# Kernel tuning notes

Hardware: AMD Instinct MI355X
Metric: run time of the kernel (lower is better)

## Reference

```python
import jax, jax.numpy as jnp
import numpy as np

N = 100000      # nodes
E = 3200000     # edges (avg degree 32)
FEA = 67
HID = 16
OUT = 2
K = 3           # num_stacks
T = 2           # num_layers


def setup_inputs() -> dict:
    key = jax.random.key(0)
    ks = jax.random.split(key, 11)
    s = 0.1  # weight init scale
    return {
        "x": jax.random.normal(ks[0], (N, FEA), jnp.float32),
        "edge_index": jax.random.randint(ks[1], (2, E), 0, N, dtype=jnp.int32),
        "init_w1": jax.random.normal(ks[2], (K, FEA, HID), jnp.float32) * s,
        "w1": jax.random.normal(ks[3], (1, K, HID, HID), jnp.float32) * s,
        "root_w1": jax.random.normal(ks[4], (1, K, FEA, HID), jnp.float32) * s,
        "b1": jax.random.normal(ks[5], (1, K, 1, HID), jnp.float32) * s,
        "init_w2": jax.random.normal(ks[6], (K, HID, OUT), jnp.float32) * s,
        "w2": jax.random.normal(ks[7], (1, K, OUT, OUT), jnp.float32) * s,
        "root_w2": jax.random.normal(ks[8], (1, K, HID, OUT), jnp.float32) * s,
        "b2": jax.random.normal(ks[9], (1, K, 1, OUT), jnp.float32) * s,
    }


def gcn_norm(src, dst, n):
    # symmetric normalization of A WITHOUT self-loops (PyG ARMAConv behavior)
    deg = jax.ops.segment_sum(jnp.ones(src.shape[0], jnp.float32), dst, num_segments=n)
    dinv = jnp.where(deg > 0, jax.lax.rsqrt(jnp.maximum(deg, 1.0)), 0.0)
    return dinv[src] * dinv[dst]  # [E]


def arma_conv(x, src, dst, norm, init_w, w, root_w, bias, act, n):
    # x: [N, Fin]; shared_weights=True, num_layers=T, num_stacks=K
    out = jnp.einsum('nf,kfh->knh', x, init_w)           # t=0 transform
    root = jnp.einsum('nf,kfh->knh', x, root_w[0])       # root term (dropout=identity in eval)
    for t in range(T):
        if t > 0:
            out = jnp.einsum('knh,khp->knp', out, w[0])
        # propagate: out[i] = sum_{(j->i)} norm_e * out[j]
        m = (out[:, src, :] * norm[None, :, None]).transpose(1, 0, 2)  # [E,K,H]
        agg = jax.ops.segment_sum(m, dst, num_segments=n).transpose(1, 0, 2)  # [K,N,H]
        out = agg + root + bias[0]
        if act:
            out = jax.nn.relu(out)
    return out.mean(axis=0)  # average over stacks -> [N, H]


def reference(x, edge_index, init_w1, w1, root_w1, b1, init_w2, w2, root_w2, b2):
    src, dst = edge_index[0], edge_index[1]
    n = x.shape[0]
    norm = gcn_norm(src, dst, n)
    h = jax.nn.relu(arma_conv(x, src, dst, norm, init_w1, w1, root_w1, b1, True, n))
    o = arma_conv(h, src, dst, norm, init_w2, w2, root_w2, b2, False, n)
    return jax.nn.log_softmax(o, axis=1)
```

## Files before the change

### kernel.cpp

```cpp
#include <hip/hip_runtime.h>
#include <hip/hip_fp16.h>
#include <math.h>

#define NN 100000
#define NE 3200000
#define FEA 67
#define HID 16
#define OUTC 2
#define KS 3
#define KH 48
#define KO 6
#define PAD 64

#define PB 512
#define EPB 6250
#define BINW 512
#define NBINS 196
#define M1 (NBINS * PB)
#define NSCB 98
#define CSR_CAP (NE + NBINS * 3 * BINW + 64)

#define TBM 128
#define TNB ((NN + TBM - 1) / TBM)
#define XS_STRIDE 132
#define WT_STRIDE 68


__global__ void k_hist(const int* __restrict__ dst, int* __restrict__ hist) {
    __shared__ int h[NBINS];
    if (threadIdx.x < NBINS) h[threadIdx.x] = 0;
    __syncthreads();
    int base = blockIdx.x * EPB;
    for (int i = threadIdx.x; i < EPB; i += 256)
        atomicAdd(&h[dst[base + i] >> 9], 1);
    __syncthreads();
    if (threadIdx.x < NBINS) hist[threadIdx.x * PB + blockIdx.x] = h[threadIdx.x];
}


__global__ void k_partial(const int* __restrict__ in, int* __restrict__ partials, int n) {
    __shared__ int s[256];
    int base = blockIdx.x * 1024;
    int acc = 0;
    for (int i = threadIdx.x; i < 1024; i += 256) {
        int idx = base + i;
        if (idx < n) acc += in[idx];
    }
    s[threadIdx.x] = acc;
    __syncthreads();
    for (int off = 128; off > 0; off >>= 1) {
        if (threadIdx.x < off) s[threadIdx.x] += s[threadIdx.x + off];
        __syncthreads();
    }
    if (threadIdx.x == 0) partials[blockIdx.x] = s[0];
}

__global__ void k_downsweepF(const int* __restrict__ in, const int* __restrict__ partials,
                             int* __restrict__ out, int n) {
    __shared__ int ps[256];
    __shared__ int s[256];
    int t = threadIdx.x;
    ps[t] = (t < NSCB) ? partials[t] : 0;
    __syncthreads();
    for (int off = 1; off < 256; off <<= 1) {
        int v = (t >= off) ? ps[t - off] : 0;
        __syncthreads();
        ps[t] += v;
        __syncthreads();
    }
    int bbase = (blockIdx.x > 0) ? ps[blockIdx.x - 1] : 0;

    int base = blockIdx.x * 1024 + t * 4;
    int d0 = 0, d1 = 0, d2 = 0, d3 = 0;
    if (base + 0 < n) d0 = in[base + 0];
    if (base + 1 < n) d1 = in[base + 1];
    if (base + 2 < n) d2 = in[base + 2];
    if (base + 3 < n) d3 = in[base + 3];
    int ts = d0 + d1 + d2 + d3;
    s[t] = ts;
    __syncthreads();
    for (int off = 1; off < 256; off <<= 1) {
        int v = (t >= off) ? s[t - off] : 0;
        __syncthreads();
        s[t] += v;
        __syncthreads();
    }
    int excl = s[t] - ts + bbase;
    if (base + 0 < n) out[base + 0] = excl;
    if (base + 1 < n) out[base + 1] = excl + d0;
    if (base + 2 < n) out[base + 2] = excl + d0 + d1;
    if (base + 3 < n) out[base + 3] = excl + d0 + d1 + d2;
}


__global__ void k_pass2(const int* __restrict__ src, const int* __restrict__ dst,
                        const int* __restrict__ hist_scan, int* __restrict__ recs) {
    __shared__ int curs[NBINS];
    if (threadIdx.x < NBINS) curs[threadIdx.x] = hist_scan[threadIdx.x * PB + blockIdx.x];
    __syncthreads();
    int base = blockIdx.x * EPB;
    for (int i = threadIdx.x; i < EPB; i += 256) {
        int e = base + i;
        int s = src[e], d = dst[e];
        int pos = atomicAdd(&curs[d >> 9], 1);
        recs[pos] = s | ((d & 511) << 17);
    }
}


__global__ void k_degsort(const int* __restrict__ recs, const int* __restrict__ hist_scan,
                          int* __restrict__ deg, float* __restrict__ dinv,
                          int* __restrict__ row_start, int* __restrict__ csr) {
    __shared__ int cnt[BINW];
    __shared__ int scn[BINW];
    int bin = blockIdx.x, t = threadIdx.x;
    cnt[t] = 0;
    __syncthreads();
    int s0 = hist_scan[bin * PB];
    int s1 = (bin + 1 < NBINS) ? hist_scan[(bin + 1) * PB] : NE;
    for (int r = s0 + t; r < s1; r += BINW)
        atomicAdd(&cnt[((unsigned)recs[r]) >> 17], 1);
    __syncthreads();
    int c  = cnt[t];
    int c4 = (c + 3) & ~3;
    scn[t] = c4;
    __syncthreads();
    for (int off = 1; off < BINW; off <<= 1) {
        int v = (t >= off) ? scn[t - off] : 0;
        __syncthreads();
        scn[t] += v;
        __syncthreads();
    }
    int base = s0 + bin * (3 * BINW);
    int rs   = base + scn[t] - c4;
    int node = bin * BINW + t;
    if (node < NN) {
        deg[node]       = c;
        dinv[node]      = (c > 0) ? rsqrtf((float)c) : 0.f;
        row_start[node] = rs;
    }
    scn[t] = rs;
    __syncthreads();
    for (int r = s0 + t; r < s1; r += BINW) {
        int rec = recs[r];
        int pos = atomicAdd(&scn[((unsigned)rec) >> 17], 1);
        csr[pos] = rec & 0x1FFFF;
    }
    __syncthreads();
    int e4 = rs + c4;
    for (int i = scn[t]; i < e4; ++i) csr[i] = NN;
}


__global__ void k_transform1(const float* __restrict__ x, const float* __restrict__ iw,
                             const float* __restrict__ rw, const float* __restrict__ b1,
                             const float* __restrict__ dinv,
                             __half* __restrict__ A, __half* __restrict__ Bpad,
                             __half2* __restrict__ Rh) {
    if (blockIdx.x == TNB) {
        int t = threadIdx.x;
        if (t < PAD) A[(size_t)NN * PAD + t] = __float2half(0.f);
        else if (t < 2 * PAD) Bpad[(size_t)NN * PAD + (t - PAD)] = __float2half(0.f);
        return;
    }
    __shared__ float xs[FEA * XS_STRIDE];
    __shared__ float wTs[96 * WT_STRIDE];
    __shared__ float bb[KH];
    int n0g = blockIdx.x * TBM;

    for (int idx = threadIdx.x; idx < 96 * FEA; idx += 256) {
        int j = idx / FEA, f = idx % FEA;
        float v;
        if (j < KH) v = iw[(j >> 4) * (FEA * HID) + f * HID + (j & 15)];
        else { int jr = j - KH; v = rw[(jr >> 4) * (FEA * HID) + f * HID + (jr & 15)]; }
        wTs[j * WT_STRIDE + f] = v;
    }
    if (threadIdx.x < KH) bb[threadIdx.x] = b1[threadIdx.x];
    for (int idx = threadIdx.x; idx < TBM * FEA; idx += 256) {
        int nl = idx / FEA, f = idx % FEA;
        int n = n0g + nl;
        xs[f * XS_STRIDE + nl] = (n < NN) ? x[(size_t)n * FEA + f] : 0.f;
    }
    __syncthreads();

    int tx = threadIdx.x & 31, ty = threadIdx.x >> 5;
    int nl0 = tx * 4;
    int j0  = ty * 12;
    float acc[4][12];
    #pragma unroll
    for (int p = 0; p < 12; ++p) {
        float init = (j0 >= KH) ? bb[j0 - KH + p] : 0.f;
        acc[0][p] = init; acc[1][p] = init; acc[2][p] = init; acc[3][p] = init;
    }

    #pragma unroll 4
    for (int fb = 0; fb < 16; ++fb) {
        int f0 = fb * 4;
        float4 xv0 = *(const float4*)&xs[(f0 + 0) * XS_STRIDE + nl0];
        float4 xv1 = *(const float4*)&xs[(f0 + 1) * XS_STRIDE + nl0];
        float4 xv2 = *(const float4*)&xs[(f0 + 2) * XS_STRIDE + nl0];
        float4 xv3 = *(const float4*)&xs[(f0 + 3) * XS_STRIDE + nl0];
        #pragma unroll
        for (int p = 0; p < 12; ++p) {
            float4 wv = *(const float4*)&wTs[(j0 + p) * WT_STRIDE + f0];
            acc[0][p] += xv0.x * wv.x + xv1.x * wv.y + xv2.x * wv.z + xv3.x * wv.w;
            acc[1][p] += xv0.y * wv.x + xv1.y * wv.y + xv2.y * wv.z + xv3.y * wv.w;
            acc[2][p] += xv0.z * wv.x + xv1.z * wv.y + xv2.z * wv.z + xv3.z * wv.w;
            acc[3][p] += xv0.w * wv.x + xv1.w * wv.y + xv2.w * wv.z + xv3.w * wv.w;
        }
    }
    #pragma unroll
    for (int f = 64; f < FEA; ++f) {
        float x0 = xs[f * XS_STRIDE + nl0 + 0];
        float x1 = xs[f * XS_STRIDE + nl0 + 1];
        float x2 = xs[f * XS_STRIDE + nl0 + 2];
        float x3 = xs[f * XS_STRIDE + nl0 + 3];
        #pragma unroll
        for (int p = 0; p < 12; ++p) {
            float wv = wTs[(j0 + p) * WT_STRIDE + f];
            acc[0][p] += x0 * wv; acc[1][p] += x1 * wv;
            acc[2][p] += x2 * wv; acc[3][p] += x3 * wv;
        }
    }

    if (j0 < KH) {
        #pragma unroll
        for (int nq = 0; nq < 4; ++nq) {
            int n = n0g + nl0 + nq;
            if (n < NN) {
                float dv = dinv[n];
                __half2* Ap = (__half2*)A + (size_t)n * (PAD / 2) + (j0 >> 1);
                #pragma unroll
                for (int p2 = 0; p2 < 6; ++p2)
                    Ap[p2] = __halves2half2(__float2half_rn(acc[nq][2 * p2] * dv),
                                            __float2half_rn(acc[nq][2 * p2 + 1] * dv));
            }
        }
    } else {
        int jh = (j0 - KH) >> 1;
        #pragma unroll
        for (int nq = 0; nq < 4; ++nq) {
            int n = n0g + nl0 + nq;
            if (n < NN) {
                __half2* Rp = Rh + (size_t)n * 24 + jh;
                #pragma unroll
                for (int p2 = 0; p2 < 6; ++p2)
                    Rp[p2] = __halves2half2(__float2half_rn(acc[nq][2 * p2]),
                                            __float2half_rn(acc[nq][2 * p2 + 1]));
            }
        }
    }
}


template <bool FUSEW>
__global__ void k_spmm48(const __half2* __restrict__ Asrc,
                         const __half2* __restrict__ Rh,
                         const int* __restrict__ row_start, const int* __restrict__ deg,
                         const float* __restrict__ dinv, const int* __restrict__ csr,
                         const float* __restrict__ w1, __half2* __restrict__ Bout) {
    __shared__ float w1s[FUSEW ? KS * HID * HID : 1];
    if (FUSEW) {
        for (int i = threadIdx.x; i < KS * HID * HID; i += 256) w1s[i] = w1[i];
        __syncthreads();
    }
    int node = (blockIdx.x * 256 + threadIdx.x) >> 6;
    int lane = threadIdx.x & 63;
    int eo   = lane >> 5;
    int cl   = lane & 31;
    int start = __builtin_amdgcn_readfirstlane(row_start[node]);
    int d     = __builtin_amdgcn_readfirstlane(deg[node]);
    int d4    = (d + 3) & ~3;
    float dv  = dinv[node];
    float2 r2 = make_float2(0.f, 0.f);
    if (cl < 24) r2 = __half22float2(Rh[(size_t)node * 24 + cl]);

    float ax = 0.f, ay = 0.f;
    for (int b = 0; b < d4; b += 64) {
        int nb  = min(64, d4 - b);
        int myc = csr[start + b + lane];
        int npf = nb >> 1;
        int p = 0;
        for (; p + 4 <= npf; p += 4) {
            int c0 = __shfl(myc, 2 * (p + 0) + eo, 64);
            int c1 = __shfl(myc, 2 * (p + 1) + eo, 64);
            int c2 = __shfl(myc, 2 * (p + 2) + eo, 64);
            int c3 = __shfl(myc, 2 * (p + 3) + eo, 64);
            float2 f0 = __half22float2(Asrc[(size_t)c0 * (PAD / 2) + cl]);
            float2 f1 = __half22float2(Asrc[(size_t)c1 * (PAD / 2) + cl]);
            float2 f2 = __half22float2(Asrc[(size_t)c2 * (PAD / 2) + cl]);
            float2 f3 = __half22float2(Asrc[(size_t)c3 * (PAD / 2) + cl]);
            ax += f0.x + f1.x; ay += f0.y + f1.y;
            ax += f2.x + f3.x; ay += f2.y + f3.y;
        }
        for (; p < npf; ++p) {
            int c = __shfl(myc, 2 * p + eo, 64);
            float2 f = __half22float2(Asrc[(size_t)c * (PAD / 2) + cl]);
            ax += f.x; ay += f.y;
        }
    }
    ax += __shfl_xor(ax, 32, 64);
    ay += __shfl_xor(ay, 32, 64);
    float vx = fmaxf(ax * dv + r2.x, 0.f);
    float vy = fmaxf(ay * dv + r2.y, 0.f);

    if (FUSEW) {
        int k  = cl >> 3;
        int p0 = (2 * cl) & 15;
        float o0 = 0.f, o1 = 0.f;
        #pragma unroll
        for (int h2 = 0; h2 < 8; ++h2) {
            float ix = __shfl(vx, k * 8 + h2, 64);
            float iy = __shfl(vy, k * 8 + h2, 64);
            o0 += ix * w1s[k * 256 + (2 * h2) * 16 + p0]     + iy * w1s[k * 256 + (2 * h2 + 1) * 16 + p0];
            o1 += ix * w1s[k * 256 + (2 * h2) * 16 + p0 + 1] + iy * w1s[k * 256 + (2 * h2 + 1) * 16 + p0 + 1];
        }
        if (eo == 0 && cl < 24)
            Bout[(size_t)node * (PAD / 2) + cl] =
                __halves2half2(__float2half_rn(o0 * dv), __float2half_rn(o1 * dv));
    } else {
        if (eo == 0 && cl < 24)
            Bout[(size_t)node * (PAD / 2) + cl] =
                __halves2half2(__float2half_rn(vx), __float2half_rn(vy));
    }
}


__global__ void k_mt2(const __half* __restrict__ L1, const float* __restrict__ iw,
                      const float* __restrict__ rw, const float* __restrict__ b2,
                      const float* __restrict__ dinv,
                      float* __restrict__ A2, float* __restrict__ R2) {
    __shared__ float wi[KS * HID * OUTC];
    __shared__ float wr_[KS * HID * OUTC];
    __shared__ float bb[KO];
    if (threadIdx.x < KS * HID * OUTC) { wi[threadIdx.x] = iw[threadIdx.x]; wr_[threadIdx.x] = rw[threadIdx.x]; }
    if (threadIdx.x < KO) bb[threadIdx.x] = b2[threadIdx.x];
    __syncthreads();
    int n = blockIdx.x * 256 + threadIdx.x;
    if (n >= NN) return;
    const __half2* hp = (const __half2*)(L1 + (size_t)n * PAD);
    float v[KH];
    #pragma unroll
    for (int q = 0; q < 24; ++q) {
        float2 f = __half22float2(hp[q]);
        v[q * 2 + 0] = f.x; v[q * 2 + 1] = f.y;
    }
    float h[HID];
    #pragma unroll
    for (int hh = 0; hh < HID; ++hh)
        h[hh] = fmaxf((v[hh] + v[16 + hh] + v[32 + hh]) * (1.f / 3.f), 0.f);
    float dv = dinv[n];
    #pragma unroll
    for (int k = 0; k < KS; ++k) {
        #pragma unroll
        for (int o = 0; o < OUTC; ++o) {
            float a = 0.f, r = bb[k * 2 + o];
            #pragma unroll
            for (int hh = 0; hh < HID; ++hh) {
                a += h[hh] * wi[k * 32 + hh * 2 + o];
                r += h[hh] * wr_[k * 32 + hh * 2 + o];
            }
            A2[n * KO + k * 2 + o] = a * dv;
            R2[n * KO + k * 2 + o] = r;
        }
    }
}


__global__ void k_spmm6_g(const float* __restrict__ Asrc, const float* __restrict__ R2,
                          const int* __restrict__ row_start, const int* __restrict__ deg,
                          const float* __restrict__ dinv, const int* __restrict__ csr,
                          const float* __restrict__ w2, float* __restrict__ Bout) {
    __shared__ float ws[KS * OUTC * OUTC];
    if (threadIdx.x < KS * OUTC * OUTC) ws[threadIdx.x] = w2[threadIdx.x];
    __syncthreads();
    int t = blockIdx.x * 256 + threadIdx.x;
    int node = t / KO, j = t % KO;
    bool active = node < NN;
    float acc = 0.f, r = 0.f, dv = 0.f;
    int start = 0, d = 0;
    if (active) {
        start = row_start[node];
        d     = deg[node];
        r     = R2[node * KO + j];
        dv    = dinv[node];
    }
    int e = 0;
    for (; e + 4 <= d; e += 4) {
        int c0 = csr[start + e + 0];
        int c1 = csr[start + e + 1];
        int c2 = csr[start + e + 2];
        int c3 = csr[start + e + 3];
        acc += Asrc[c0 * KO + j];
        acc += Asrc[c1 * KO + j];
        acc += Asrc[c2 * KO + j];
        acc += Asrc[c3 * KO + j];
    }
    for (; e < d; ++e)
        acc += Asrc[csr[start + e] * KO + j];
    float v = acc * dv + r;
    float other = __shfl_xor(v, 1, 64);
    if (active) {
        int k = j >> 1, p = j & 1;
        float v0 = (p == 0) ? v : other;
        float v1 = (p == 0) ? other : v;
        Bout[node * KO + j] = (v0 * ws[k * 4 + p] + v1 * ws[k * 4 + 2 + p]) * dv;
    }
}


__global__ void k_spmm6_f(const float* __restrict__ Asrc, const float* __restrict__ R2,
                          const int* __restrict__ row_start, const int* __restrict__ deg,
                          const float* __restrict__ dinv, const int* __restrict__ csr,
                          float* __restrict__ out) {
    int wave = threadIdx.x >> 6;
    int l    = threadIdx.x & 63;
    int nl   = l / 6;
    int j    = l - nl * 6;
    bool active = nl < 10;
    int node = blockIdx.x * 40 + wave * 10 + nl;
    float acc = 0.f, r = 0.f, dv = 0.f;
    int start = 0, d = 0;
    if (active) {
        start = row_start[node];
        d     = deg[node];
        r     = R2[node * KO + j];
        dv    = dinv[node];
    }
    int e = 0;
    for (; e + 4 <= d; e += 4) {
        int c0 = csr[start + e + 0];
        int c1 = csr[start + e + 1];
        int c2 = csr[start + e + 2];
        int c3 = csr[start + e + 3];
        acc += Asrc[c0 * KO + j];
        acc += Asrc[c1 * KO + j];
        acc += Asrc[c2 * KO + j];
        acc += Asrc[c3 * KO + j];
    }
    for (; e < d; ++e)
        acc += Asrc[csr[start + e] * KO + j];
    float v = acc * dv + r;
    int base = nl * 6;
    float o0 = (__shfl(v, base + 0, 64) + __shfl(v, base + 2, 64) + __shfl(v, base + 4, 64)) * (1.f / 3.f);
    float o1 = (__shfl(v, base + 1, 64) + __shfl(v, base + 3, 64) + __shfl(v, base + 5, 64)) * (1.f / 3.f);
    if (active && j == 0) {
        float m = fmaxf(o0, o1);
        float ls = m + logf(expf(o0 - m) + expf(o1 - m));
        *(float2*)(out + (size_t)node * 2) = make_float2(o0 - ls, o1 - ls);
    }
}


extern "C" void kernel_launch(void* const* d_in, const int* in_sizes, int n_in,
                              void* d_out, int out_size, void* d_ws, size_t ws_size,
                              hipStream_t stream) {
    const float* x   = (const float*)d_in[0];
    const int*   ei  = (const int*)d_in[1];
    const float* iw1 = (const float*)d_in[2];
    const float* w1  = (const float*)d_in[3];
    const float* rw1 = (const float*)d_in[4];
    const float* b1  = (const float*)d_in[5];
    const float* iw2 = (const float*)d_in[6];
    const float* w2  = (const float*)d_in[7];
    const float* rw2 = (const float*)d_in[8];
    const float* b2  = (const float*)d_in[9];
    const int* src = ei;
    const int* dst = ei + NE;
    float* out = (float*)d_out;

    char* ws = (char*)d_ws;
    size_t o = 0;
    int*     deg       = (int*)(ws + o);     o += (size_t)NN * 4;
    int*     row_start = (int*)(ws + o);     o += (size_t)NN * 4;
    float*   dinv      = (float*)(ws + o);   o += (size_t)NN * 4;
    int*     hist      = (int*)(ws + o);     o += (size_t)M1 * 4;
    int*     hist_scan = (int*)(ws + o);     o += (size_t)M1 * 4;
    int*     partials  = (int*)(ws + o);     o += 128 * 4;
    int*     csr       = (int*)(ws + o);     o += (size_t)CSR_CAP * 4;
    __half*  A         = (__half*)(ws + o);  o += (size_t)(NN + 1) * PAD * 2;
    __half2* Rh        = (__half2*)(ws + o); o += (size_t)NN * 24 * 4;
    __half*  B         = (__half*)(ws + o);  o += (size_t)(NN + 1) * PAD * 2;
    int*    recs  = (int*)A;
    __half* L1f   = A;
    float*  A2    = (float*)Rh;
    float*  R2    = (float*)Rh + (size_t)NN * KO;
    float*  C2    = (float*)Rh + (size_t)NN * KO * 2;

    k_hist       <<<PB, 256, 0, stream>>>(dst, hist);
    k_partial    <<<NSCB, 256, 0, stream>>>(hist, partials, M1);
    k_downsweepF <<<NSCB, 256, 0, stream>>>(hist, partials, hist_scan, M1);
    k_pass2      <<<PB, 256, 0, stream>>>(src, dst, hist_scan, recs);
    k_degsort    <<<NBINS, BINW, 0, stream>>>(recs, hist_scan, deg, dinv, row_start, csr);

    k_transform1    <<<TNB + 1, 256, 0, stream>>>(x, iw1, rw1, b1, dinv, A, B, Rh);
    k_spmm48<true>  <<<NN / 4, 256, 0, stream>>>((const __half2*)A, Rh, row_start, deg, dinv, csr, w1, (__half2*)B);
    k_spmm48<false> <<<NN / 4, 256, 0, stream>>>((const __half2*)B, Rh, row_start, deg, dinv, csr, w1, (__half2*)L1f);

    k_mt2      <<<(NN + 255) / 256, 256, 0, stream>>>(L1f, iw2, rw2, b2, dinv, A2, R2);
    k_spmm6_g  <<<(NN * KO + 255) / 256, 256, 0, stream>>>(A2, R2, row_start, deg, dinv, csr, w2, C2);
    k_spmm6_f  <<<NN / 40, 256, 0, stream>>>(C2, R2, row_start, deg, dinv, csr, out);
}
```

Baseline: 324.0 us.

## Split layer-1 features into per-stack planar arrays and run SpMM per stack

Replaces the 64-half padded per-node layout holding all three stacks with three planar 16-half arrays, and launches the first-layer SpMM once per stack with 8 lanes per neighbour and 8 neighbours per step. CSR rows are padded to multiples of 8 to match. This removes the wasted padding lanes and shrinks the per-launch gather working set for better cache hit rates, at the cost of traversing the CSR three times and more kernel launches.

```diff
diff --git a/kernel.cpp b/kernel.cpp
--- a/kernel.cpp
+++ b/kernel.cpp
@@ -10,7 +10,6 @@
 #define KS 3
 #define KH 48
 #define KO 6
-#define PAD 64
 
 #define PB 512
 #define EPB 6250
@@ -18,12 +17,15 @@
 #define NBINS 196
 #define M1 (NBINS * PB)
 #define NSCB 98
-#define CSR_CAP (NE + NBINS * 3 * BINW + 64)
+#define CSR_CAP (NE + NBINS * 7 * BINW + 64)
 
 #define TBM 128
 #define TNB ((NN + TBM - 1) / TBM)
 #define XS_STRIDE 132
 #define WT_STRIDE 68
+
+#define APS ((size_t)(NN + 1) * 8)
+#define RPS ((size_t)NN * 8)
 
 
 __global__ void k_hist(const int* __restrict__ dst, int* __restrict__ hist) {
@@ -122,8 +124,8 @@
         atomicAdd(&cnt[((unsigned)recs[r]) >> 17], 1);
     __syncthreads();
     int c  = cnt[t];
-    int c4 = (c + 3) & ~3;
-    scn[t] = c4;
+    int c8 = (c + 7) & ~7;
+    scn[t] = c8;
     __syncthreads();
     for (int off = 1; off < BINW; off <<= 1) {
         int v = (t >= off) ? scn[t - off] : 0;
@@ -131,8 +133,8 @@
         scn[t] += v;
         __syncthreads();
     }
-    int base = s0 + bin * (3 * BINW);
-    int rs   = base + scn[t] - c4;
+    int base = s0 + bin * (7 * BINW);
+    int rs   = base + scn[t] - c8;
     int node = bin * BINW + t;
     if (node < NN) {
         deg[node]       = c;
@@ -147,20 +149,21 @@
         csr[pos] = rec & 0x1FFFF;
     }
     __syncthreads();
-    int e4 = rs + c4;
-    for (int i = scn[t]; i < e4; ++i) csr[i] = NN;
+    int e8 = rs + c8;
+    for (int i = scn[t]; i < e8; ++i) csr[i] = NN;
 }
 
 
 __global__ void k_transform1(const float* __restrict__ x, const float* __restrict__ iw,
                              const float* __restrict__ rw, const float* __restrict__ b1,
                              const float* __restrict__ dinv,
-                             __half* __restrict__ A, __half* __restrict__ Bpad,
-                             __half2* __restrict__ Rh) {
+                             __half2* __restrict__ Ap, __half2* __restrict__ Bp,
+                             __half2* __restrict__ Rp) {
     if (blockIdx.x == TNB) {
         int t = threadIdx.x;
-        if (t < PAD) A[(size_t)NN * PAD + t] = __float2half(0.f);
-        else if (t < 2 * PAD) Bpad[(size_t)NN * PAD + (t - PAD)] = __float2half(0.f);
+        __half2 z = __halves2half2(__float2half(0.f), __float2half(0.f));
+        if (t < 24)      Ap[(size_t)(t >> 3) * APS + (size_t)NN * 8 + (t & 7)] = z;
+        else if (t < 48) Bp[(size_t)((t - 24) >> 3) * APS + (size_t)NN * 8 + ((t - 24) & 7)] = z;
         return;
     }
     __shared__ float xs[FEA * XS_STRIDE];
@@ -229,24 +232,28 @@
             int n = n0g + nl0 + nq;
             if (n < NN) {
                 float dv = dinv[n];
-                __half2* Ap = (__half2*)A + (size_t)n * (PAD / 2) + (j0 >> 1);
                 #pragma unroll
-                for (int p2 = 0; p2 < 6; ++p2)
-                    Ap[p2] = __halves2half2(__float2half_rn(acc[nq][2 * p2] * dv),
-                                            __float2half_rn(acc[nq][2 * p2 + 1] * dv));
+                for (int p2 = 0; p2 < 6; ++p2) {
+                    int jp = j0 + 2 * p2;
+                    Ap[(size_t)(jp >> 4) * APS + (size_t)n * 8 + ((jp & 15) >> 1)] =
+                        __halves2half2(__float2half_rn(acc[nq][2 * p2] * dv),
+                                       __float2half_rn(acc[nq][2 * p2 + 1] * dv));
+                }
             }
         }
     } else {
-        int jh = (j0 - KH) >> 1;
+        int jr0 = j0 - KH;
         #pragma unroll
         for (int nq = 0; nq < 4; ++nq) {
             int n = n0g + nl0 + nq;
             if (n < NN) {
-                __half2* Rp = Rh + (size_t)n * 24 + jh;
                 #pragma unroll
-                for (int p2 = 0; p2 < 6; ++p2)
-                    Rp[p2] = __halves2half2(__float2half_rn(acc[nq][2 * p2]),
-                                            __float2half_rn(acc[nq][2 * p2 + 1]));
+                for (int p2 = 0; p2 < 6; ++p2) {
+                    int jp = jr0 + 2 * p2;
+                    Rp[(size_t)(jp >> 4) * RPS + (size_t)n * 8 + ((jp & 15) >> 1)] =
+                        __halves2half2(__float2half_rn(acc[nq][2 * p2]),
+                                       __float2half_rn(acc[nq][2 * p2 + 1]));
+                }
             }
         }
     }
@@ -254,79 +261,79 @@
 
 
 template <bool FUSEW>
-__global__ void k_spmm48(const __half2* __restrict__ Asrc,
-                         const __half2* __restrict__ Rh,
+__global__ void k_spmm16(const __half2* __restrict__ Ak,
+                         const __half2* __restrict__ Rk,
                          const int* __restrict__ row_start, const int* __restrict__ deg,
                          const float* __restrict__ dinv, const int* __restrict__ csr,
-                         const float* __restrict__ w1, __half2* __restrict__ Bout) {
-    __shared__ float w1s[FUSEW ? KS * HID * HID : 1];
+                         const float* __restrict__ w1k,
+                         __half2* __restrict__ Bk) {
+    __shared__ float w1s[FUSEW ? HID * HID : 1];
     if (FUSEW) {
-        for (int i = threadIdx.x; i < KS * HID * HID; i += 256) w1s[i] = w1[i];
+        if (threadIdx.x < HID * HID) w1s[threadIdx.x] = w1k[threadIdx.x];
         __syncthreads();
     }
     int node = (blockIdx.x * 256 + threadIdx.x) >> 6;
     int lane = threadIdx.x & 63;
-    int eo   = lane >> 5;
-    int cl   = lane & 31;
+    int eo   = lane >> 3;
+    int cl   = lane & 7;
     int start = __builtin_amdgcn_readfirstlane(row_start[node]);
     int d     = __builtin_amdgcn_readfirstlane(deg[node]);
-    int d4    = (d + 3) & ~3;
+    int d8    = (d + 7) & ~7;
     float dv  = dinv[node];
-    float2 r2 = make_float2(0.f, 0.f);
-    if (cl < 24) r2 = __half22float2(Rh[(size_t)node * 24 + cl]);
+    float2 r2 = __half22float2(Rk[(size_t)node * 8 + cl]);
 
     float ax = 0.f, ay = 0.f;
-    for (int b = 0; b < d4; b += 64) {
-        int nb  = min(64, d4 - b);
+    for (int b = 0; b < d8; b += 64) {
+        int nb  = min(64, d8 - b);
         int myc = csr[start + b + lane];
-        int npf = nb >> 1;
+        int npf = nb >> 3;
         int p = 0;
         for (; p + 4 <= npf; p += 4) {
-            int c0 = __shfl(myc, 2 * (p + 0) + eo, 64);
-            int c1 = __shfl(myc, 2 * (p + 1) + eo, 64);
-            int c2 = __shfl(myc, 2 * (p + 2) + eo, 64);
-            int c3 = __shfl(myc, 2 * (p + 3) + eo, 64);
-            float2 f0 = __half22float2(Asrc[(size_t)c0 * (PAD / 2) + cl]);
-            float2 f1 = __half22float2(Asrc[(size_t)c1 * (PAD / 2) + cl]);
-            float2 f2 = __half22float2(Asrc[(size_t)c2 * (PAD / 2) + cl]);
-            float2 f3 = __half22float2(Asrc[(size_t)c3 * (PAD / 2) + cl]);
+            int c0 = __shfl(myc, (p + 0) * 8 + eo, 64);
+            int c1 = __shfl(myc, (p + 1) * 8 + eo, 64);
+            int c2 = __shfl(myc, (p + 2) * 8 + eo, 64);
+            int c3 = __shfl(myc, (p + 3) * 8 + eo, 64);
+            float2 f0 = __half22float2(Ak[((size_t)c0 << 3) + cl]);
+            float2 f1 = __half22float2(Ak[((size_t)c1 << 3) + cl]);
+            float2 f2 = __half22float2(Ak[((size_t)c2 << 3) + cl]);
+            float2 f3 = __half22float2(Ak[((size_t)c3 << 3) + cl]);
             ax += f0.x + f1.x; ay += f0.y + f1.y;
             ax += f2.x + f3.x; ay += f2.y + f3.y;
         }
         for (; p < npf; ++p) {
-            int c = __shfl(myc, 2 * p + eo, 64);
-            float2 f = __half22float2(Asrc[(size_t)c * (PAD / 2) + cl]);
+            int c = __shfl(myc, p * 8 + eo, 64);
+            float2 f = __half22float2(Ak[((size_t)c << 3) + cl]);
             ax += f.x; ay += f.y;
         }
     }
-    ax += __shfl_xor(ax, 32, 64);
-    ay += __shfl_xor(ay, 32, 64);
+    ax += __shfl_xor(ax, 8, 64);  ay += __shfl_xor(ay, 8, 64);
+    ax += __shfl_xor(ax, 16, 64); ay += __shfl_xor(ay, 16, 64);
+    ax += __shfl_xor(ax, 32, 64); ay += __shfl_xor(ay, 32, 64);
     float vx = fmaxf(ax * dv + r2.x, 0.f);
     float vy = fmaxf(ay * dv + r2.y, 0.f);
 
     if (FUSEW) {
-        int k  = cl >> 3;
-        int p0 = (2 * cl) & 15;
+        int p0 = 2 * cl;
         float o0 = 0.f, o1 = 0.f;
         #pragma unroll
         for (int h2 = 0; h2 < 8; ++h2) {
-            float ix = __shfl(vx, k * 8 + h2, 64);
-            float iy = __shfl(vy, k * 8 + h2, 64);
-            o0 += ix * w1s[k * 256 + (2 * h2) * 16 + p0]     + iy * w1s[k * 256 + (2 * h2 + 1) * 16 + p0];
-            o1 += ix * w1s[k * 256 + (2 * h2) * 16 + p0 + 1] + iy * w1s[k * 256 + (2 * h2 + 1) * 16 + p0 + 1];
-        }
-        if (eo == 0 && cl < 24)
-            Bout[(size_t)node * (PAD / 2) + cl] =
+            float ix = __shfl(vx, h2, 64);
+            float iy = __shfl(vy, h2, 64);
+            o0 += ix * w1s[(2 * h2) * 16 + p0]     + iy * w1s[(2 * h2 + 1) * 16 + p0];
+            o1 += ix * w1s[(2 * h2) * 16 + p0 + 1] + iy * w1s[(2 * h2 + 1) * 16 + p0 + 1];
+        }
+        if (eo == 0)
+            Bk[(size_t)node * 8 + cl] =
                 __halves2half2(__float2half_rn(o0 * dv), __float2half_rn(o1 * dv));
     } else {
-        if (eo == 0 && cl < 24)
-            Bout[(size_t)node * (PAD / 2) + cl] =
+        if (eo == 0)
+            Bk[(size_t)node * 8 + cl] =
                 __halves2half2(__float2half_rn(vx), __float2half_rn(vy));
     }
 }
 
 
-__global__ void k_mt2(const __half* __restrict__ L1, const float* __restrict__ iw,
+__global__ void k_mt2(const __half2* __restrict__ L1, const float* __restrict__ iw,
                       const float* __restrict__ rw, const float* __restrict__ b2,
                       const float* __restrict__ dinv,
                       float* __restrict__ A2, float* __restrict__ R2) {
@@ -338,17 +345,15 @@
     __syncthreads();
     int n = blockIdx.x * 256 + threadIdx.x;
     if (n >= NN) return;
-    const __half2* hp = (const __half2*)(L1 + (size_t)n * PAD);
-    float v[KH];
-    #pragma unroll
-    for (int q = 0; q < 24; ++q) {
-        float2 f = __half22float2(hp[q]);
-        v[q * 2 + 0] = f.x; v[q * 2 + 1] = f.y;
-    }
     float h[HID];
     #pragma unroll
-    for (int hh = 0; hh < HID; ++hh)
-        h[hh] = fmaxf((v[hh] + v[16 + hh] + v[32 + hh]) * (1.f / 3.f), 0.f);
+    for (int q = 0; q < 8; ++q) {
+        float2 f0 = __half22float2(L1[(size_t)n * 8 + q]);
+        float2 f1 = __half22float2(L1[APS + (size_t)n * 8 + q]);
+        float2 f2 = __half22float2(L1[2 * APS + (size_t)n * 8 + q]);
+        h[2 * q + 0] = fmaxf((f0.x + f1.x + f2.x) * (1.f / 3.f), 0.f);
+        h[2 * q + 1] = fmaxf((f0.y + f1.y + f2.y) * (1.f / 3.f), 0.f);
+    }
     float dv = dinv[n];
     #pragma unroll
     for (int k = 0; k < KS; ++k) {
@@ -478,14 +483,14 @@
     int*     hist_scan = (int*)(ws + o);     o += (size_t)M1 * 4;
     int*     partials  = (int*)(ws + o);     o += 128 * 4;
     int*     csr       = (int*)(ws + o);     o += (size_t)CSR_CAP * 4;
-    __half*  A         = (__half*)(ws + o);  o += (size_t)(NN + 1) * PAD * 2;
-    __half2* Rh        = (__half2*)(ws + o); o += (size_t)NN * 24 * 4;
-    __half*  B         = (__half*)(ws + o);  o += (size_t)(NN + 1) * PAD * 2;
-    int*    recs  = (int*)A;
-    __half* L1f   = A;
-    float*  A2    = (float*)Rh;
-    float*  R2    = (float*)Rh + (size_t)NN * KO;
-    float*  C2    = (float*)Rh + (size_t)NN * KO * 2;
+    __half2* Ap        = (__half2*)(ws + o); o += 3 * APS * 4;
+    __half2* Rp        = (__half2*)(ws + o); o += 3 * RPS * 4;
+    __half2* Bp        = (__half2*)(ws + o); o += 3 * APS * 4;
+    int*    recs  = (int*)Ap;
+    __half2* L1f  = Ap;
+    float*  A2    = (float*)Rp;
+    float*  R2    = (float*)Rp + (size_t)NN * KO;
+    float*  C2    = (float*)Rp + (size_t)NN * KO * 2;
 
     k_hist       <<<PB, 256, 0, stream>>>(dst, hist);
     k_partial    <<<NSCB, 256, 0, stream>>>(hist, partials, M1);
@@ -493,11 +498,17 @@
     k_pass2      <<<PB, 256, 0, stream>>>(src, dst, hist_scan, recs);
     k_degsort    <<<NBINS, BINW, 0, stream>>>(recs, hist_scan, deg, dinv, row_start, csr);
 
-    k_transform1    <<<TNB + 1, 256, 0, stream>>>(x, iw1, rw1, b1, dinv, A, B, Rh);
-    k_spmm48<true>  <<<NN / 4, 256, 0, stream>>>((const __half2*)A, Rh, row_start, deg, dinv, csr, w1, (__half2*)B);
-    k_spmm48<false> <<<NN / 4, 256, 0, stream>>>((const __half2*)B, Rh, row_start, deg, dinv, csr, w1, (__half2*)L1f);
-
-    k_mt2      <<<(NN + 255) / 256, 256, 0, stream>>>(L1f, iw2, rw2, b2, dinv, A2, R2);
-    k_spmm6_g  <<<(NN * KO + 255) / 256, 256, 0, stream>>>(A2, R2, row_start, deg, dinv, csr, w2, C2);
-    k_spmm6_f  <<<NN / 40, 256, 0, stream>>>(C2, R2, row_start, deg, dinv, csr, out);
-}
+    k_transform1 <<<TNB + 1, 256, 0, stream>>>(x, iw1, rw1, b1, dinv, Ap, Bp, Rp);
+    for (int k = 0; k < KS; ++k)
+        k_spmm16<true><<<NN / 4, 256, 0, stream>>>(Ap + k * APS, Rp + k * RPS,
+                                                   row_start, deg, dinv, csr,
+                                                   w1 + k * 256, Bp + k * APS);
+    for (int k = 0; k < KS; ++k)
+        k_spmm16<false><<<NN / 4, 256, 0, stream>>>(Bp + k * APS, Rp + k * RPS,
+                                                    row_start, deg, dinv, csr,
+                                                    w1, L1f + k * APS);
+
+    k_mt2     <<<(NN + 255) / 256, 256, 0, stream>>>(L1f, iw2, rw2, b2, dinv, A2, R2);
+    k_spmm6_g <<<(NN * KO + 255) / 256, 256, 0, stream>>>(A2, R2, row_start, deg, dinv, csr, w2, C2);
+    k_spmm6_f <<<NN / 40, 256, 0, stream>>>(C2, R2, row_start, deg, dinv, csr, out);
+}
```

New measurement: 433.2 us. +33.7%, slower.

## Split first-layer transform into weight-prep kernel and 2D-gridded node-tile GEMM

Applied to the files above, without the earlier changes.

Moves the weight transpose out of every block into a one-block prep kernel that writes a pre-transposed weight matrix to workspace. The transform then runs on a 2D grid: 64-node tiles, with the init half and the root half computed by separate blocks. Each thread computes 12 outputs for one node, and x rows are staged row-major with coalesced loads. This raises parallelism and cuts per-block staging cost, but adds a kernel launch and lowers register reuse (1 node per thread instead of 4).

```diff
diff --git a/kernel.cpp b/kernel.cpp
--- a/kernel.cpp
+++ b/kernel.cpp
@@ -20,10 +20,7 @@
 #define NSCB 98
 #define CSR_CAP (NE + NBINS * 3 * BINW + 64)
 
-#define TBM 128
-#define TNB ((NN + TBM - 1) / TBM)
-#define XS_STRIDE 132
-#define WT_STRIDE 68
+#define T1B 1563
 
 
 __global__ void k_hist(const int* __restrict__ dst, int* __restrict__ hist) {
@@ -152,102 +149,84 @@
 }
 
 
-__global__ void k_transform1(const float* __restrict__ x, const float* __restrict__ iw,
-                             const float* __restrict__ rw, const float* __restrict__ b1,
-                             const float* __restrict__ dinv,
-                             __half* __restrict__ A, __half* __restrict__ Bpad,
-                             __half2* __restrict__ Rh) {
-    if (blockIdx.x == TNB) {
-        int t = threadIdx.x;
-        if (t < PAD) A[(size_t)NN * PAD + t] = __float2half(0.f);
-        else if (t < 2 * PAD) Bpad[(size_t)NN * PAD + (t - PAD)] = __float2half(0.f);
-        return;
-    }
-    __shared__ float xs[FEA * XS_STRIDE];
-    __shared__ float wTs[96 * WT_STRIDE];
-    __shared__ float bb[KH];
-    int n0g = blockIdx.x * TBM;
-
-    for (int idx = threadIdx.x; idx < 96 * FEA; idx += 256) {
-        int j = idx / FEA, f = idx % FEA;
-        float v;
-        if (j < KH) v = iw[(j >> 4) * (FEA * HID) + f * HID + (j & 15)];
-        else { int jr = j - KH; v = rw[(jr >> 4) * (FEA * HID) + f * HID + (jr & 15)]; }
-        wTs[j * WT_STRIDE + f] = v;
-    }
-    if (threadIdx.x < KH) bb[threadIdx.x] = b1[threadIdx.x];
-    for (int idx = threadIdx.x; idx < TBM * FEA; idx += 256) {
-        int nl = idx / FEA, f = idx % FEA;
-        int n = n0g + nl;
-        xs[f * XS_STRIDE + nl] = (n < NN) ? x[(size_t)n * FEA + f] : 0.f;
-    }
-    __syncthreads();
-
-    int tx = threadIdx.x & 31, ty = threadIdx.x >> 5;
-    int nl0 = tx * 4;
-    int j0  = ty * 12;
-    float acc[4][12];
+__global__ void k_wprep(const float* __restrict__ iw, const float* __restrict__ rw,
+                        float* __restrict__ wT, __half2* __restrict__ Ah, __half2* __restrict__ Bh) {
+    int t = threadIdx.x;
+    __half2 z = __halves2half2(__float2half(0.f), __float2half(0.f));
+    if (t < 32)      Ah[(size_t)NN * 32 + t] = z;
+    else if (t < 64) Bh[(size_t)NN * 32 + (t - 32)] = z;
+    for (int idx = t; idx < KS * FEA * HID; idx += 256) {
+        int k = idx / (FEA * HID);
+        int r = idx - k * (FEA * HID);
+        int f = r >> 4, h = r & 15;
+        int j = k * 16 + h;
+        float vi = iw[idx], vr = rw[idx];
+        wT[j * 68 + f]        = vi;
+        wT[(48 + j) * 68 + f] = vr;
+    }
+}
+
+
+__global__ void k_t1(const float* __restrict__ x, const float* __restrict__ wT,
+                     const float* __restrict__ b1, const float* __restrict__ dinv,
+                     __half2* __restrict__ Ah, __half2* __restrict__ Rh) {
+    __shared__ float xs[64 * 68];
+    __shared__ float wls[48 * 68];
+    __shared__ float bbs[48];
+    int half = blockIdx.y;
+    int n0   = blockIdx.x * 64;
+    const float* wsrc = wT + half * (48 * 68);
+    for (int idx = threadIdx.x; idx < 48 * 68; idx += 256) wls[idx] = wsrc[idx];
+    for (int idx = threadIdx.x; idx < 64 * FEA; idx += 256) {
+        int nl = idx / FEA, f = idx - nl * FEA;
+        int n = n0 + nl;
+        xs[nl * 68 + f] = (n < NN) ? x[(size_t)n0 * FEA + idx] : 0.f;
+    }
+    if (half && threadIdx.x < 48) bbs[threadIdx.x] = b1[threadIdx.x];
+    __syncthreads();
+
+    int nl = threadIdx.x >> 2, cg = threadIdx.x & 3;
+    int n  = n0 + nl;
+    float acc[12];
     #pragma unroll
-    for (int p = 0; p < 12; ++p) {
-        float init = (j0 >= KH) ? bb[j0 - KH + p] : 0.f;
-        acc[0][p] = init; acc[1][p] = init; acc[2][p] = init; acc[3][p] = init;
-    }
-
+    for (int p = 0; p < 12; ++p) acc[p] = 0.f;
+    if (half) {
+        #pragma unroll
+        for (int p = 0; p < 12; ++p) acc[p] = bbs[cg * 12 + p];
+    }
+    const float* xr = &xs[nl * 68];
+    const float* wb = &wls[cg * 12 * 68];
     #pragma unroll 4
     for (int fb = 0; fb < 16; ++fb) {
         int f0 = fb * 4;
-        float4 xv0 = *(const float4*)&xs[(f0 + 0) * XS_STRIDE + nl0];
-        float4 xv1 = *(const float4*)&xs[(f0 + 1) * XS_STRIDE + nl0];
-        float4 xv2 = *(const float4*)&xs[(f0 + 2) * XS_STRIDE + nl0];
-        float4 xv3 = *(const float4*)&xs[(f0 + 3) * XS_STRIDE + nl0];
+        float4 xv = *(const float4*)&xr[f0];
         #pragma unroll
         for (int p = 0; p < 12; ++p) {
-            float4 wv = *(const float4*)&wTs[(j0 + p) * WT_STRIDE + f0];
-            acc[0][p] += xv0.x * wv.x + xv1.x * wv.y + xv2.x * wv.z + xv3.x * wv.w;
-            acc[1][p] += xv0.y * wv.x + xv1.y * wv.y + xv2.y * wv.z + xv3.y * wv.w;
-            acc[2][p] += xv0.z * wv.x + xv1.z * wv.y + xv2.z * wv.z + xv3.z * wv.w;
-            acc[3][p] += xv0.w * wv.x + xv1.w * wv.y + xv2.w * wv.z + xv3.w * wv.w;
+            float4 wv = *(const float4*)&wb[p * 68 + f0];
+            acc[p] += xv.x * wv.x + xv.y * wv.y + xv.z * wv.z + xv.w * wv.w;
         }
     }
     #pragma unroll
     for (int f = 64; f < FEA; ++f) {
-        float x0 = xs[f * XS_STRIDE + nl0 + 0];
-        float x1 = xs[f * XS_STRIDE + nl0 + 1];
-        float x2 = xs[f * XS_STRIDE + nl0 + 2];
-        float x3 = xs[f * XS_STRIDE + nl0 + 3];
+        float xv = xr[f];
         #pragma unroll
-        for (int p = 0; p < 12; ++p) {
-            float wv = wTs[(j0 + p) * WT_STRIDE + f];
-            acc[0][p] += x0 * wv; acc[1][p] += x1 * wv;
-            acc[2][p] += x2 * wv; acc[3][p] += x3 * wv;
-        }
-    }
-
-    if (j0 < KH) {
-        #pragma unroll
-        for (int nq = 0; nq < 4; ++nq) {
-            int n = n0g + nl0 + nq;
-            if (n < NN) {
-                float dv = dinv[n];
-                __half2* Ap = (__half2*)A + (size_t)n * (PAD / 2) + (j0 >> 1);
-                #pragma unroll
-                for (int p2 = 0; p2 < 6; ++p2)
-                    Ap[p2] = __halves2half2(__float2half_rn(acc[nq][2 * p2] * dv),
-                                            __float2half_rn(acc[nq][2 * p2 + 1] * dv));
-            }
-        }
-    } else {
-        int jh = (j0 - KH) >> 1;
-        #pragma unroll
-        for (int nq = 0; nq < 4; ++nq) {
-            int n = n0g + nl0 + nq;
-            if (n < NN) {
-                __half2* Rp = Rh + (size_t)n * 24 + jh;
-                #pragma unroll
-                for (int p2 = 0; p2 < 6; ++p2)
-                    Rp[p2] = __halves2half2(__float2half_rn(acc[nq][2 * p2]),
-                                            __float2half_rn(acc[nq][2 * p2 + 1]));
-            }
+        for (int p = 0; p < 12; ++p) acc[p] += xv * wb[p * 68 + f];
+    }
+
+    if (n < NN) {
+        if (half == 0) {
+            float dv = dinv[n];
+            #pragma unroll
+            for (int p2 = 0; p2 < 6; ++p2)
+                Ah[(size_t)n * 32 + cg * 6 + p2] =
+                    __halves2half2(__float2half_rn(acc[2 * p2] * dv),
+                                   __float2half_rn(acc[2 * p2 + 1] * dv));
+        } else {
+            #pragma unroll
+            for (int p2 = 0; p2 < 6; ++p2)
+                Rh[(size_t)n * 24 + cg * 6 + p2] =
+                    __halves2half2(__float2half_rn(acc[2 * p2]),
+                                   __float2half_rn(acc[2 * p2 + 1]));
         }
     }
 }
@@ -481,6 +460,7 @@
     __half*  A         = (__half*)(ws + o);  o += (size_t)(NN + 1) * PAD * 2;
     __half2* Rh        = (__half2*)(ws + o); o += (size_t)NN * 24 * 4;
     __half*  B         = (__half*)(ws + o);  o += (size_t)(NN + 1) * PAD * 2;
+    float*   wT        = (float*)(ws + o);   o += 96 * 68 * 4;
     int*    recs  = (int*)A;
     __half* L1f   = A;
     float*  A2    = (float*)Rh;
@@ -493,11 +473,12 @@
     k_pass2      <<<PB, 256, 0, stream>>>(src, dst, hist_scan, recs);
     k_degsort    <<<NBINS, BINW, 0, stream>>>(recs, hist_scan, deg, dinv, row_start, csr);
 
-    k_transform1    <<<TNB + 1, 256, 0, stream>>>(x, iw1, rw1, b1, dinv, A, B, Rh);
+    k_wprep <<<1, 256, 0, stream>>>(iw1, rw1, wT, (__half2*)A, (__half2*)B);
+    k_t1    <<<dim3(T1B, 2), 256, 0, stream>>>(x, wT, b1, dinv, (__half2*)A, Rh);
     k_spmm48<true>  <<<NN / 4, 256, 0, stream>>>((const __half2*)A, Rh, row_start, deg, dinv, csr, w1, (__half2*)B);
     k_spmm48<false> <<<NN / 4, 256, 0, stream>>>((const __half2*)B, Rh, row_start, deg, dinv, csr, w1, (__half2*)L1f);
 
-    k_mt2      <<<(NN + 255) / 256, 256, 0, stream>>>(L1f, iw2, rw2, b2, dinv, A2, R2);
-    k_spmm6_g  <<<(NN * KO + 255) / 256, 256, 0, stream>>>(A2, R2, row_start, deg, dinv, csr, w2, C2);
-    k_spmm6_f  <<<NN / 40, 256, 0, stream>>>(C2, R2, row_start, deg, dinv, csr, out);
-}
+    k_mt2     <<<(NN + 255) / 256, 256, 0, stream>>>(L1f, iw2, rw2, b2, dinv, A2, R2);
+    k_spmm6_g <<<(NN * KO + 255) / 256, 256, 0, stream>>>(A2, R2, row_start, deg, dinv, csr, w2, C2);
+    k_spmm6_f <<<NN / 40, 256, 0, stream>>>(C2, R2, row_start, deg, dinv, csr, out);
+}
```

Result: no change. 319.3 us (-1.4%).
